# Optimization experiments

Measured on AMD Instinct MI355X. Metric: run time of the kernel, lower is better.

## Reference

```python
import jax, jax.numpy as jnp
import numpy as np

TOP_K = 4


def setup_inputs() -> dict:
    key = jax.random.key(0)
    k1, k2, k3 = jax.random.split(key, 3)
    tokens, hidden_dim, num_experts = 16384, 2880, 128
    hidden_states = jax.random.normal(k1, (tokens, hidden_dim), dtype=jnp.float32)
    weight = jax.random.normal(k2, (num_experts, hidden_dim), dtype=jnp.float32) * 0.02
    bias = jax.random.normal(k3, (num_experts,), dtype=jnp.float32) * 0.02
    return {"hidden_states": hidden_states, "weight": weight, "bias": bias}


def reference(hidden_states, weight, bias):
    # hidden_states: [T, H]; weight: [E, H]; bias: [E]
    x = hidden_states.reshape(-1, weight.shape[1])
    router_logits = jnp.einsum("th,eh->te", x, weight) + bias  # [T, E]
    router_top_value, router_indices = jax.lax.top_k(router_logits, TOP_K)  # [T, K]
    router_top_value = jax.nn.softmax(router_top_value, axis=-1)
    return router_top_value, router_indices, router_logits
```

## Files before the change

### kernel.cpp

```cpp
#include <hip/hip_runtime.h>
#include <math.h>

#define H       2880
#define H4      720
#define NTOK    16384
#define NEXP    128
#define NCHUNK  90
#define NSTEP   180
#define GAP_EPS 1e-3f

typedef __attribute__((ext_vector_type(8)))  short bf16x8;
typedef __attribute__((ext_vector_type(16))) float f32x16;

union FragU { unsigned int u[4]; bf16x8 v; };

__device__ inline bf16x8 pack_hi2(float4 a, float4 b) {
    const float f[8] = {a.x,a.y,a.z,a.w,b.x,b.y,b.z,b.w};
    FragU r;
#pragma unroll
    for (int j = 0; j < 4; ++j) {
        unsigned u0 = __float_as_uint(f[2*j]);
        unsigned u1 = __float_as_uint(f[2*j+1]);
        r.u[j] = (u1 & 0xFFFF0000u) | (u0 >> 16);
    }
    return r.v;
}
__device__ inline bf16x8 pack_lo2(float4 a, float4 b) {
    const float f[8] = {a.x,a.y,a.z,a.w,b.x,b.y,b.z,b.w};
    FragU r;
#pragma unroll
    for (int j = 0; j < 4; ++j) {
        float x0 = f[2*j],   h0 = __uint_as_float(__float_as_uint(x0) & 0xFFFF0000u);
        float x1 = f[2*j+1], h1 = __uint_as_float(__float_as_uint(x1) & 0xFFFF0000u);
        unsigned l0 = __float_as_uint(x0 - h0);
        unsigned l1 = __float_as_uint(x1 - h1);
        r.u[j] = (l1 & 0xFFFF0000u) | (l0 >> 16);
    }
    return r.v;
}

__global__ __launch_bounds__(256) void wconv(
    const float* __restrict__ w, short* __restrict__ whiF, short* __restrict__ wloF)
{
    const int gid = blockIdx.x * 256 + threadIdx.x;
    const int l   = gid & 63;
    const int nt  = (gid >> 6) & 3;
    const int s   = gid >> 8;
    const int e   = nt * 32 + (l & 31);
    const int k0  = s * 16 + (l >> 5) * 8;
    const float4* wp = (const float4*)(w + (size_t)e * H + k0);
    const float4 a = wp[0], b = wp[1];
    *(bf16x8*)(whiF + (size_t)gid * 8) = pack_hi2(a, b);
    *(bf16x8*)(wloF + (size_t)gid * 8) = pack_lo2(a, b);
}

__global__ __launch_bounds__(64, 2) void router_gemm_mfma(
    const float* __restrict__ x,
    const short* __restrict__ whiF,
    const short* __restrict__ wloF,
    float* __restrict__ p0,
    float* __restrict__ pws)
{
    __shared__ float xs[3][1024];

    const int lane = threadIdx.x;
    const int bm   = blockIdx.x;
    const int z    = blockIdx.y;
    const int ks   = gridDim.y;
    const int t0   = bm * 32;

    const int base2 = (NCHUNK / ks) & ~1;
    const int pairs = (NCHUNK - base2 * ks) >> 1;
    const int c0 = z * base2 + 2 * (z < pairs ? z : pairs);
    const int c1 = c0 + base2 + (z < pairs ? 2 : 0);

    float* outp = (z == 0) ? p0 : (pws + (size_t)(z - 1) * NTOK * NEXP);

    const float4* gs = (const float4*)x + (size_t)(t0 + (lane >> 3)) * H4 + ((lane & 7) ^ (lane >> 3));
    const unsigned xsb = (unsigned)(uintptr_t)&xs[0][0];
    const int r31 = lane & 31, lx7 = lane & 7, kh2 = (lane >> 5) * 2;

    f32x16 acc[4];
#pragma unroll
    for (int nt = 0; nt < 4; ++nt)
#pragma unroll
        for (int r = 0; r < 16; ++r) acc[nt][r] = 0.0f;

    bf16x8 bA[16], bB[16];

#define GL(SRC, DST) __builtin_amdgcn_global_load_lds(                                   \
        (const __attribute__((address_space(1))) void*)(SRC),                            \
        (__attribute__((address_space(3))) void*)(DST), 16, 0, 0)

#define STAGE(SB, CC) {                                                                  \
    const float4* g_ = gs + (size_t)(CC) * 8;                                            \
    GL(g_,                  &xs[SB][0]);                                                 \
    GL(g_ + (size_t) 8*H4,  &xs[SB][256]);                                               \
    GL(g_ + (size_t)16*H4,  &xs[SB][512]);                                               \
    GL(g_ + (size_t)24*H4,  &xs[SB][768]); }

#define BLOAD_ST(DST, CC, ST) {                                                          \
    _Pragma("unroll")                                                                    \
    for (int nt = 0; nt < 4; ++nt) {                                                     \
        const size_t o_ = ((size_t)(((CC)*2 + (ST))*4 + nt)*64 + lane) * 8;              \
        DST[(ST)*8 + nt*2]     = *(const bf16x8*)(whiF + o_);                            \
        DST[(ST)*8 + nt*2 + 1] = *(const bf16x8*)(wloF + o_); } }

#define MFMA_HALF(BANK, ST, AH, AL) {                                                    \
    _Pragma("unroll")                                                                    \
    for (int nt = 0; nt < 4; ++nt) {                                                     \
        acc[nt] = __builtin_amdgcn_mfma_f32_32x32x16_bf16(AH, BANK[(ST)*8 + nt*2],     acc[nt], 0,0,0); \
        acc[nt] = __builtin_amdgcn_mfma_f32_32x32x16_bf16(AL, BANK[(ST)*8 + nt*2],     acc[nt], 0,0,0); \
        acc[nt] = __builtin_amdgcn_mfma_f32_32x32x16_bf16(AH, BANK[(ST)*8 + nt*2 + 1], acc[nt], 0,0,0); } }

#define DSREAD_PACK(BUF, AH0, AL0, AH1, AL1) {                                           \
    const unsigned ab  = xsb + (unsigned)(BUF) * 4096u + (unsigned)r31 * 128u;           \
    const unsigned a00 = ab + 16u * (unsigned)((kh2    ) ^ lx7);                         \
    const unsigned a01 = ab + 16u * (unsigned)((kh2 + 1) ^ lx7);                         \
    const unsigned a10 = ab + 16u * (unsigned)((kh2 + 4) ^ lx7);                         \
    const unsigned a11 = ab + 16u * (unsigned)((kh2 + 5) ^ lx7);                         \
    float4 q0, q1, q2, q3;                                                               \
    asm volatile("ds_read_b128 %0, %1" : "=v"(q0) : "v"(a00) : "memory");                \
    asm volatile("ds_read_b128 %0, %1" : "=v"(q1) : "v"(a01) : "memory");                \
    asm volatile("ds_read_b128 %0, %1" : "=v"(q2) : "v"(a10) : "memory");                \
    asm volatile("ds_read_b128 %0, %1" : "=v"(q3) : "v"(a11) : "memory");                \
    asm volatile("s_waitcnt lgkmcnt(0)" ::: "memory");                                   \
    __builtin_amdgcn_sched_barrier(0);                                                   \
    AH0 = pack_hi2(q0, q1); AL0 = pack_lo2(q0, q1);                                      \
    AH1 = pack_hi2(q2, q3); AL1 = pack_lo2(q2, q3); }

    STAGE(0, c0);
    STAGE(1, c0 + 1);
    BLOAD_ST(bA, c0, 0);     BLOAD_ST(bA, c0, 1);
    BLOAD_ST(bB, c0 + 1, 0); BLOAD_ST(bB, c0 + 1, 1);

    int rb = 0;
    bf16x8 ah0, al0, ah1, al1;
    for (int c = c0; c < c1 - 2; c += 2) {
        const int sb  = (rb + 2 >= 3) ? rb - 1 : rb + 2;
        const int rb1 = (rb + 1 >= 3) ? 0 : rb + 1;
        STAGE(sb, c + 2);
        asm volatile("s_waitcnt vmcnt(40)" ::: "memory");
        DSREAD_PACK(rb, ah0, al0, ah1, al1);
        MFMA_HALF(bA, 0, ah0, al0);
        BLOAD_ST(bA, c + 2, 0);
        MFMA_HALF(bA, 1, ah1, al1);
        BLOAD_ST(bA, c + 2, 1);
        STAGE(rb, c + 3);
        asm volatile("s_waitcnt vmcnt(40)" ::: "memory");
        DSREAD_PACK(rb1, ah0, al0, ah1, al1);
        MFMA_HALF(bB, 0, ah0, al0);
        BLOAD_ST(bB, c + 3, 0);
        MFMA_HALF(bB, 1, ah1, al1);
        BLOAD_ST(bB, c + 3, 1);
        rb = (rb >= 1) ? rb - 1 : 2;
    }
    {
        const int rb1 = (rb + 1 >= 3) ? 0 : rb + 1;
        asm volatile("s_waitcnt vmcnt(36)" ::: "memory");
        DSREAD_PACK(rb, ah0, al0, ah1, al1);
        MFMA_HALF(bA, 0, ah0, al0);
        MFMA_HALF(bA, 1, ah1, al1);
        asm volatile("s_waitcnt vmcnt(16)" ::: "memory");
        DSREAD_PACK(rb1, ah0, al0, ah1, al1);
        MFMA_HALF(bB, 0, ah0, al0);
        MFMA_HALF(bB, 1, ah1, al1);
    }

    const int ecol  = lane & 31;
    const int rbase = t0 + 4 * (lane >> 5);
#pragma unroll
    for (int nt = 0; nt < 4; ++nt)
#pragma unroll
        for (int r = 0; r < 16; ++r) {
            const int orow = rbase + (r & 3) + 8 * (r >> 2);
            outp[(size_t)orow * NEXP + nt * 32 + ecol] = acc[nt][r];
        }
}

__global__ __launch_bounds__(256) void reduce_cand(
    float* __restrict__ p0,
    const float* __restrict__ pws,
    const float* __restrict__ bias,
    int* __restrict__ cand,
    float* __restrict__ vals,
    float* __restrict__ inds,
    int ks)
{
    const int tid = threadIdx.x;
    const int tok = blockIdx.x * 8 + (tid >> 5);
    const int l   = tid & 31;

    float4* row = (float4*)p0 + (size_t)tok * 32 + l;
    float4 s = row[0];
    for (int zz = 1; zz < ks; ++zz) {
        const float4 pz = ((const float4*)(pws + (size_t)(zz - 1) * NTOK * NEXP))[(size_t)tok * 32 + l];
        s.x += pz.x; s.y += pz.y; s.z += pz.z; s.w += pz.w;
    }
    const float4 bb = ((const float4*)bias)[l];
    s.x += bb.x; s.y += bb.y; s.z += bb.z; s.w += bb.w;
    row[0] = s;

    float v[4] = {s.x, s.y, s.z, s.w};
    float vv[8]; int out[8];
#pragma unroll
    for (int r = 0; r < 8; ++r) {
        float lv = v[0]; int lj = 0;
#pragma unroll
        for (int j = 1; j < 4; ++j) if (v[j] > lv) { lv = v[j]; lj = j; }
        int le = l * 4 + lj;
#pragma unroll
        for (int m = 1; m < 32; m <<= 1) {
            const float ov = __shfl_xor(lv, m, 32);
            const int   oe = __shfl_xor(le, m, 32);
            if (ov > lv || (ov == lv && oe < le)) { lv = ov; le = oe; }
        }
        vv[r] = lv; out[r] = le;
        if ((le >> 2) == l) v[le & 3] = -3.4e38f;
    }

    float ming = vv[0] - vv[1];
    ming = fminf(ming, vv[1] - vv[2]);
    ming = fminf(ming, vv[2] - vv[3]);
    ming = fminf(ming, vv[3] - vv[4]);
    const bool slow = (ming < GAP_EPS);

    if (l == 0) {
        int4 o0 = {out[0] | (slow ? (1 << 30) : 0), out[1], out[2], out[3]};
        int4 o1 = {out[4], out[5], out[6], out[7]};
        *(int4*)(cand + (size_t)tok * 8)     = o0;
        *(int4*)(cand + (size_t)tok * 8 + 4) = o1;
        if (!slow) {
            const float e1 = expf(vv[1] - vv[0]);
            const float e2 = expf(vv[2] - vv[0]);
            const float e3 = expf(vv[3] - vv[0]);
            const float sm = 1.0f + e1 + e2 + e3;
            float4 ov = {1.0f / sm, e1 / sm, e2 / sm, e3 / sm};
            float4 oi = {(float)out[0], (float)out[1], (float)out[2], (float)out[3]};
            *(float4*)(&vals[(size_t)tok * 4]) = ov;
            *(float4*)(&inds[(size_t)tok * 4]) = oi;
        }
    }
}

__global__ __launch_bounds__(256) void fixup_topk(
    const float* __restrict__ x,
    const float* __restrict__ w,
    const float* __restrict__ bias,
    const int* __restrict__ cand,
    float* __restrict__ vals,
    float* __restrict__ inds)
{
    const int lane = threadIdx.x & 63;
    const int wv   = threadIdx.x >> 6;
    const int tok  = blockIdx.x * 4 + wv;

    const int head = cand[(size_t)tok * 8];
    if (!(head & (1 << 30))) return;

    const int c    = lane >> 3;
    const int s    = lane & 7;
    const int cidx = cand[(size_t)tok * 8 + c] & 0x3fffffff;

    const float4* xr = (const float4*)x + (size_t)tok  * H4;
    const float4* wr = (const float4*)w + (size_t)cidx * H4;

    double acc = 0.0;
    for (int j = 0; j < 90; ++j) {
        const float4 a = xr[s + 8 * j];
        const float4 b = wr[s + 8 * j];
        acc = fma((double)a.x, (double)b.x, acc);
        acc = fma((double)a.y, (double)b.y, acc);
        acc = fma((double)a.z, (double)b.z, acc);
        acc = fma((double)a.w, (double)b.w, acc);
    }
    acc += __shfl_xor(acc, 1);
    acc += __shfl_xor(acc, 2);
    acc += __shfl_xor(acc, 4);
    const double exact = acc + (double)bias[cidx];

    double bv[8]; int bidx[8];
#pragma unroll
    for (int g = 0; g < 8; ++g) { bv[g] = __shfl(exact, g * 8); bidx[g] = __shfl(cidx, g * 8); }

    float fv[4]; int fi[4];
#pragma unroll
    for (int k = 0; k < 4; ++k) {
        double best = -1.0e300; int bi = 1 << 30; int bg = -1;
#pragma unroll
        for (int g = 0; g < 8; ++g) {
            if (bv[g] > best || (bv[g] == best && bidx[g] < bi)) { best = bv[g]; bi = bidx[g]; bg = g; }
        }
#pragma unroll
        for (int g = 0; g < 8; ++g) if (g == bg) bv[g] = -1.0e300;
        fv[k] = (float)best; fi[k] = bi;
    }

    if (lane == 0) {
        const float e1 = expf(fv[1] - fv[0]);
        const float e2 = expf(fv[2] - fv[0]);
        const float e3 = expf(fv[3] - fv[0]);
        const float sm = 1.0f + e1 + e2 + e3;
        float4 ov = {1.0f / sm, e1 / sm, e2 / sm, e3 / sm};
        float4 oi = {(float)fi[0], (float)fi[1], (float)fi[2], (float)fi[3]};
        *(float4*)(&vals[(size_t)tok * 4]) = ov;
        *(float4*)(&inds[(size_t)tok * 4]) = oi;
    }
}

extern "C" void kernel_launch(void* const* d_in, const int* in_sizes, int n_in,
                              void* d_out, int out_size, void* d_ws, size_t ws_size,
                              hipStream_t stream) {
    const float* x    = (const float*)d_in[0];
    const float* w    = (const float*)d_in[1];
    const float* bias = (const float*)d_in[2];

    float* out    = (float*)d_out;
    float* vals   = out;
    float* inds   = out + NTOK * 4;
    float* logits = out + NTOK * 8;

    const size_t WPLANE = (size_t)NEXP * H * sizeof(short);
    const size_t PB     = (size_t)NTOK * NEXP * sizeof(float);
    const size_t CB     = (size_t)NTOK * 8 * sizeof(int);

    int ks = 1;
    if      (ws_size >= 2 * WPLANE + 3 * PB + CB) ks = 4;
    else if (ws_size >= 2 * WPLANE + 1 * PB + CB) ks = 2;

    short* whiF = (short*)d_ws;
    short* wloF = whiF + (size_t)NEXP * H;
    float* pws  = (float*)(wloF + (size_t)NEXP * H);
    int*   cand = (int*)(pws + (size_t)(ks - 1) * NTOK * NEXP);

    wconv<<<NSTEP, 256, 0, stream>>>(w, whiF, wloF);
    router_gemm_mfma<<<dim3(NTOK / 32, ks), 64, 0, stream>>>(x, whiF, wloF, logits, pws);
    reduce_cand<<<NTOK / 8, 256, 0, stream>>>(logits, pws, bias, cand, vals, inds, ks);
    fixup_topk<<<NTOK / 4, 256, 0, stream>>>(x, w, bias, cand, vals, inds);
}
```

Measured before the change: 85.65 us.

## Fuse split-K reduction, bias and top-k candidate selection into the router GEMM

Split-K now runs inside one 256-thread block, four waves each covering a K range. Their partial accumulators are combined through shared memory, and wave 0 adds the bias, writes the logits and runs the top-8 candidate selection and softmax directly. This removes the global partial-sum workspace round trip and the separate reduce_cand launch. In exchange the block needs 48KB of LDS and occupancy drops, and the epilogue is serialised in one wave per 32 tokens.

```diff
diff --git a/kernel.cpp b/kernel.cpp
--- a/kernel.cpp
+++ b/kernel.cpp
@@ -7,6 +7,7 @@
 #define NEXP    128
 #define NCHUNK  90
 #define NSTEP   180
+#define KSW     4
 #define GAP_EPS 1e-3f
 
 typedef __attribute__((ext_vector_type(8)))  short bf16x8;
@@ -54,30 +55,31 @@
     *(bf16x8*)(wloF + (size_t)gid * 8) = pack_lo2(a, b);
 }
 
-__global__ __launch_bounds__(64, 2) void router_gemm_mfma(
+__global__ __launch_bounds__(256, 3) void router_gemm_fused(
     const float* __restrict__ x,
     const short* __restrict__ whiF,
     const short* __restrict__ wloF,
-    float* __restrict__ p0,
-    float* __restrict__ pws)
+    const float* __restrict__ bias,
+    float* __restrict__ logits,
+    int* __restrict__ cand,
+    float* __restrict__ vals,
+    float* __restrict__ inds)
 {
-    __shared__ float xs[3][1024];
-
-    const int lane = threadIdx.x;
+    __shared__ float xs[4][3][1024];
+
+    const int tid  = threadIdx.x;
+    const int lane = tid & 63;
+    const int wv   = tid >> 6;
     const int bm   = blockIdx.x;
-    const int z    = blockIdx.y;
-    const int ks   = gridDim.y;
     const int t0   = bm * 32;
 
-    const int base2 = (NCHUNK / ks) & ~1;
-    const int pairs = (NCHUNK - base2 * ks) >> 1;
-    const int c0 = z * base2 + 2 * (z < pairs ? z : pairs);
-    const int c1 = c0 + base2 + (z < pairs ? 2 : 0);
-
-    float* outp = (z == 0) ? p0 : (pws + (size_t)(z - 1) * NTOK * NEXP);
+    const int base2 = (NCHUNK / KSW) & ~1;
+    const int pairs = (NCHUNK - base2 * KSW) >> 1;
+    const int c0 = wv * base2 + 2 * (wv < pairs ? wv : pairs);
+    const int c1 = c0 + base2 + (wv < pairs ? 2 : 0);
 
     const float4* gs = (const float4*)x + (size_t)(t0 + (lane >> 3)) * H4 + ((lane & 7) ^ (lane >> 3));
-    const unsigned xsb = (unsigned)(uintptr_t)&xs[0][0];
+    const unsigned xsb = (unsigned)(uintptr_t)&xs[wv][0][0];
     const int r31 = lane & 31, lx7 = lane & 7, kh2 = (lane >> 5) * 2;
 
     f32x16 acc[4];
@@ -94,10 +96,10 @@
 
 #define STAGE(SB, CC) {                                                                  \
     const float4* g_ = gs + (size_t)(CC) * 8;                                            \
-    GL(g_,                  &xs[SB][0]);                                                 \
-    GL(g_ + (size_t) 8*H4,  &xs[SB][256]);                                               \
-    GL(g_ + (size_t)16*H4,  &xs[SB][512]);                                               \
-    GL(g_ + (size_t)24*H4,  &xs[SB][768]); }
+    GL(g_,                  &xs[wv][SB][0]);                                             \
+    GL(g_ + (size_t) 8*H4,  &xs[wv][SB][256]);                                           \
+    GL(g_ + (size_t)16*H4,  &xs[wv][SB][512]);                                           \
+    GL(g_ + (size_t)24*H4,  &xs[wv][SB][768]); }
 
 #define BLOAD_ST(DST, CC, ST) {                                                          \
     _Pragma("unroll")                                                                    \
@@ -167,78 +169,84 @@
         MFMA_HALF(bB, 1, ah1, al1);
     }
 
-    const int ecol  = lane & 31;
+    __syncthreads();
+    float* exch = &xs[0][0][0];
+    if (wv > 0) {
+        const int eb = (wv - 1) * 4096;
+#pragma unroll
+        for (int nt = 0; nt < 4; ++nt)
+#pragma unroll
+            for (int r = 0; r < 16; ++r)
+                exch[eb + (nt * 16 + r) * 64 + lane] = acc[nt][r];
+    }
+    __syncthreads();
+    if (wv != 0) return;
+
+#pragma unroll
+    for (int nt = 0; nt < 4; ++nt)
+#pragma unroll
+        for (int r = 0; r < 16; ++r) {
+            const int sl = (nt * 16 + r) * 64 + lane;
+            acc[nt][r] = ((acc[nt][r] + exch[sl]) + exch[4096 + sl]) + exch[8192 + sl];
+        }
+
+    const int l31 = lane & 31;
+    const float bv0 = bias[l31], bv1 = bias[32 + l31], bv2 = bias[64 + l31], bv3 = bias[96 + l31];
+#pragma unroll
+    for (int r = 0; r < 16; ++r) {
+        acc[0][r] += bv0; acc[1][r] += bv1; acc[2][r] += bv2; acc[3][r] += bv3;
+    }
+
     const int rbase = t0 + 4 * (lane >> 5);
 #pragma unroll
     for (int nt = 0; nt < 4; ++nt)
 #pragma unroll
         for (int r = 0; r < 16; ++r) {
             const int orow = rbase + (r & 3) + 8 * (r >> 2);
-            outp[(size_t)orow * NEXP + nt * 32 + ecol] = acc[nt][r];
-        }
-}
-
-__global__ __launch_bounds__(256) void reduce_cand(
-    float* __restrict__ p0,
-    const float* __restrict__ pws,
-    const float* __restrict__ bias,
-    int* __restrict__ cand,
-    float* __restrict__ vals,
-    float* __restrict__ inds,
-    int ks)
-{
-    const int tid = threadIdx.x;
-    const int tok = blockIdx.x * 8 + (tid >> 5);
-    const int l   = tid & 31;
-
-    float4* row = (float4*)p0 + (size_t)tok * 32 + l;
-    float4 s = row[0];
-    for (int zz = 1; zz < ks; ++zz) {
-        const float4 pz = ((const float4*)(pws + (size_t)(zz - 1) * NTOK * NEXP))[(size_t)tok * 32 + l];
-        s.x += pz.x; s.y += pz.y; s.z += pz.z; s.w += pz.w;
-    }
-    const float4 bb = ((const float4*)bias)[l];
-    s.x += bb.x; s.y += bb.y; s.z += bb.z; s.w += bb.w;
-    row[0] = s;
-
-    float v[4] = {s.x, s.y, s.z, s.w};
-    float vv[8]; int out[8];
-#pragma unroll
-    for (int r = 0; r < 8; ++r) {
-        float lv = v[0]; int lj = 0;
-#pragma unroll
-        for (int j = 1; j < 4; ++j) if (v[j] > lv) { lv = v[j]; lj = j; }
-        int le = l * 4 + lj;
-#pragma unroll
-        for (int m = 1; m < 32; m <<= 1) {
-            const float ov = __shfl_xor(lv, m, 32);
-            const int   oe = __shfl_xor(le, m, 32);
-            if (ov > lv || (ov == lv && oe < le)) { lv = ov; le = oe; }
-        }
-        vv[r] = lv; out[r] = le;
-        if ((le >> 2) == l) v[le & 3] = -3.4e38f;
-    }
-
-    float ming = vv[0] - vv[1];
-    ming = fminf(ming, vv[1] - vv[2]);
-    ming = fminf(ming, vv[2] - vv[3]);
-    ming = fminf(ming, vv[3] - vv[4]);
-    const bool slow = (ming < GAP_EPS);
-
-    if (l == 0) {
-        int4 o0 = {out[0] | (slow ? (1 << 30) : 0), out[1], out[2], out[3]};
-        int4 o1 = {out[4], out[5], out[6], out[7]};
-        *(int4*)(cand + (size_t)tok * 8)     = o0;
-        *(int4*)(cand + (size_t)tok * 8 + 4) = o1;
-        if (!slow) {
-            const float e1 = expf(vv[1] - vv[0]);
-            const float e2 = expf(vv[2] - vv[0]);
-            const float e3 = expf(vv[3] - vv[0]);
-            const float sm = 1.0f + e1 + e2 + e3;
-            float4 ov = {1.0f / sm, e1 / sm, e2 / sm, e3 / sm};
-            float4 oi = {(float)out[0], (float)out[1], (float)out[2], (float)out[3]};
-            *(float4*)(&vals[(size_t)tok * 4]) = ov;
-            *(float4*)(&inds[(size_t)tok * 4]) = oi;
+            logits[(size_t)orow * NEXP + nt * 32 + l31] = acc[nt][r];
+        }
+
+    for (int r = 0; r < 16; ++r) {
+        const int tok = rbase + (r & 3) + 8 * (r >> 2);
+        float v[4] = {acc[0][r], acc[1][r], acc[2][r], acc[3][r]};
+        float vv[8]; int out8[8];
+#pragma unroll
+        for (int rr = 0; rr < 8; ++rr) {
+            float lv = v[0]; int lj = 0;
+#pragma unroll
+            for (int j = 1; j < 4; ++j) if (v[j] > lv) { lv = v[j]; lj = j; }
+            int le = lj * 32 + l31;
+#pragma unroll
+            for (int m = 1; m < 32; m <<= 1) {
+                const float ov = __shfl_xor(lv, m, 32);
+                const int   oe = __shfl_xor(le, m, 32);
+                if (ov > lv || (ov == lv && oe < le)) { lv = ov; le = oe; }
+            }
+            vv[rr] = lv; out8[rr] = le;
+            if ((le & 31) == l31) v[le >> 5] = -3.4e38f;
+        }
+
+        float ming = vv[0] - vv[1];
+        ming = fminf(ming, vv[1] - vv[2]);
+        ming = fminf(ming, vv[2] - vv[3]);
+        ming = fminf(ming, vv[3] - vv[4]);
+        const bool slow = (ming < GAP_EPS);
+
+        if (l31 == 0) {
+            int4 o0 = {out8[0] | (slow ? (1 << 30) : 0), out8[1], out8[2], out8[3]};
+            int4 o1 = {out8[4], out8[5], out8[6], out8[7]};
+            *(int4*)(cand + (size_t)tok * 8)     = o0;
+            *(int4*)(cand + (size_t)tok * 8 + 4) = o1;
+            if (!slow) {
+                const float e1 = expf(vv[1] - vv[0]);
+                const float e2 = expf(vv[2] - vv[0]);
+                const float e3 = expf(vv[3] - vv[0]);
+                const float sm = 1.0f + e1 + e2 + e3;
+                float4 ov = {1.0f / sm, e1 / sm, e2 / sm, e3 / sm};
+                float4 oi = {(float)out8[0], (float)out8[1], (float)out8[2], (float)out8[3]};
+                *(float4*)(&vals[(size_t)tok * 4]) = ov;
+                *(float4*)(&inds[(size_t)tok * 4]) = oi;
+            }
         }
     }
 }
@@ -320,21 +328,12 @@
     float* inds   = out + NTOK * 4;
     float* logits = out + NTOK * 8;
 
-    const size_t WPLANE = (size_t)NEXP * H * sizeof(short);
-    const size_t PB     = (size_t)NTOK * NEXP * sizeof(float);
-    const size_t CB     = (size_t)NTOK * 8 * sizeof(int);
-
-    int ks = 1;
-    if      (ws_size >= 2 * WPLANE + 3 * PB + CB) ks = 4;
-    else if (ws_size >= 2 * WPLANE + 1 * PB + CB) ks = 2;
-
     short* whiF = (short*)d_ws;
     short* wloF = whiF + (size_t)NEXP * H;
-    float* pws  = (float*)(wloF + (size_t)NEXP * H);
-    int*   cand = (int*)(pws + (size_t)(ks - 1) * NTOK * NEXP);
+    int*   cand = (int*)(wloF + (size_t)NEXP * H);
 
     wconv<<<NSTEP, 256, 0, stream>>>(w, whiF, wloF);
-    router_gemm_mfma<<<dim3(NTOK / 32, ks), 64, 0, stream>>>(x, whiF, wloF, logits, pws);
-    reduce_cand<<<NTOK / 8, 256, 0, stream>>>(logits, pws, bias, cand, vals, inds, ks);
+    router_gemm_fused<<<NTOK / 32, 256, 0, stream>>>(
+        x, whiF, wloF, bias, logits, cand, vals, inds);
     fixup_topk<<<NTOK / 4, 256, 0, stream>>>(x, w, bias, cand, vals, inds);
 }
```

Result: slower. 302.8 us (+253.5%).

## Double the GEMM token tile to 64 rows to reuse weight fragments

Applied to the files above, without the earlier changes.

Each wave now computes 64 tokens instead of 32, with two row tiles of accumulators. Every bf16 weight fragment loaded from global memory feeds MFMAs for both tiles, which halves weight traffic per token. The LDS staging buffer, the wait counts and the output store loop are widened to match, and the grid is halved. In exchange, accumulator register use doubles, launch bounds drop to one wave per SIMD, and fewer blocks run, which reduces occupancy and latency hiding.

```diff
diff --git a/kernel.cpp b/kernel.cpp
--- a/kernel.cpp
+++ b/kernel.cpp
@@ -54,20 +54,20 @@
     *(bf16x8*)(wloF + (size_t)gid * 8) = pack_lo2(a, b);
 }
 
-__global__ __launch_bounds__(64, 2) void router_gemm_mfma(
+__global__ __launch_bounds__(64, 1) void router_gemm_mfma(
     const float* __restrict__ x,
     const short* __restrict__ whiF,
     const short* __restrict__ wloF,
     float* __restrict__ p0,
     float* __restrict__ pws)
 {
-    __shared__ float xs[3][1024];
+    __shared__ float xs[3][2048];
 
     const int lane = threadIdx.x;
     const int bm   = blockIdx.x;
     const int z    = blockIdx.y;
     const int ks   = gridDim.y;
-    const int t0   = bm * 32;
+    const int t0   = bm * 64;
 
     const int base2 = (NCHUNK / ks) & ~1;
     const int pairs = (NCHUNK - base2 * ks) >> 1;
@@ -80,11 +80,11 @@
     const unsigned xsb = (unsigned)(uintptr_t)&xs[0][0];
     const int r31 = lane & 31, lx7 = lane & 7, kh2 = (lane >> 5) * 2;
 
-    f32x16 acc[4];
-#pragma unroll
-    for (int nt = 0; nt < 4; ++nt)
-#pragma unroll
-        for (int r = 0; r < 16; ++r) acc[nt][r] = 0.0f;
+    f32x16 acc[8];
+#pragma unroll
+    for (int i = 0; i < 8; ++i)
+#pragma unroll
+        for (int r = 0; r < 16; ++r) acc[i][r] = 0.0f;
 
     bf16x8 bA[16], bB[16];
 
@@ -97,7 +97,11 @@
     GL(g_,                  &xs[SB][0]);                                                 \
     GL(g_ + (size_t) 8*H4,  &xs[SB][256]);                                               \
     GL(g_ + (size_t)16*H4,  &xs[SB][512]);                                               \
-    GL(g_ + (size_t)24*H4,  &xs[SB][768]); }
+    GL(g_ + (size_t)24*H4,  &xs[SB][768]);                                               \
+    GL(g_ + (size_t)32*H4,  &xs[SB][1024]);                                              \
+    GL(g_ + (size_t)40*H4,  &xs[SB][1280]);                                              \
+    GL(g_ + (size_t)48*H4,  &xs[SB][1536]);                                              \
+    GL(g_ + (size_t)56*H4,  &xs[SB][1792]); }
 
 #define BLOAD_ST(DST, CC, ST) {                                                          \
     _Pragma("unroll")                                                                    \
@@ -106,28 +110,30 @@
         DST[(ST)*8 + nt*2]     = *(const bf16x8*)(whiF + o_);                            \
         DST[(ST)*8 + nt*2 + 1] = *(const bf16x8*)(wloF + o_); } }
 
-#define MFMA_HALF(BANK, ST, AH, AL) {                                                    \
+#define MFMA_HALF(BANK, ST, AH0, AL0, AH1, AL1) {                                        \
     _Pragma("unroll")                                                                    \
     for (int nt = 0; nt < 4; ++nt) {                                                     \
-        acc[nt] = __builtin_amdgcn_mfma_f32_32x32x16_bf16(AH, BANK[(ST)*8 + nt*2],     acc[nt], 0,0,0); \
-        acc[nt] = __builtin_amdgcn_mfma_f32_32x32x16_bf16(AL, BANK[(ST)*8 + nt*2],     acc[nt], 0,0,0); \
-        acc[nt] = __builtin_amdgcn_mfma_f32_32x32x16_bf16(AH, BANK[(ST)*8 + nt*2 + 1], acc[nt], 0,0,0); } }
-
-#define DSREAD_PACK(BUF, AH0, AL0, AH1, AL1) {                                           \
-    const unsigned ab  = xsb + (unsigned)(BUF) * 4096u + (unsigned)r31 * 128u;           \
-    const unsigned a00 = ab + 16u * (unsigned)((kh2    ) ^ lx7);                         \
-    const unsigned a01 = ab + 16u * (unsigned)((kh2 + 1) ^ lx7);                         \
-    const unsigned a10 = ab + 16u * (unsigned)((kh2 + 4) ^ lx7);                         \
-    const unsigned a11 = ab + 16u * (unsigned)((kh2 + 5) ^ lx7);                         \
+        acc[nt] = __builtin_amdgcn_mfma_f32_32x32x16_bf16(AH0, BANK[(ST)*8 + nt*2],     acc[nt], 0,0,0); \
+        acc[nt] = __builtin_amdgcn_mfma_f32_32x32x16_bf16(AL0, BANK[(ST)*8 + nt*2],     acc[nt], 0,0,0); \
+        acc[nt] = __builtin_amdgcn_mfma_f32_32x32x16_bf16(AH0, BANK[(ST)*8 + nt*2 + 1], acc[nt], 0,0,0); \
+        acc[4+nt] = __builtin_amdgcn_mfma_f32_32x32x16_bf16(AH1, BANK[(ST)*8 + nt*2],     acc[4+nt], 0,0,0); \
+        acc[4+nt] = __builtin_amdgcn_mfma_f32_32x32x16_bf16(AL1, BANK[(ST)*8 + nt*2],     acc[4+nt], 0,0,0); \
+        acc[4+nt] = __builtin_amdgcn_mfma_f32_32x32x16_bf16(AH1, BANK[(ST)*8 + nt*2 + 1], acc[4+nt], 0,0,0); } }
+
+#define DSREAD_PACK(BUF, ST, H0, L0, H1, L1, H2, L2, H3, L3) {                           \
+    const unsigned ab  = xsb + (unsigned)(BUF) * 8192u + (unsigned)r31 * 128u;           \
+    const unsigned kq0 = (unsigned)(((ST)*4 + kh2    ) ^ lx7);                           \
+    const unsigned kq1 = (unsigned)(((ST)*4 + kh2 + 1) ^ lx7);                           \
     float4 q0, q1, q2, q3;                                                               \
-    asm volatile("ds_read_b128 %0, %1" : "=v"(q0) : "v"(a00) : "memory");                \
-    asm volatile("ds_read_b128 %0, %1" : "=v"(q1) : "v"(a01) : "memory");                \
-    asm volatile("ds_read_b128 %0, %1" : "=v"(q2) : "v"(a10) : "memory");                \
-    asm volatile("ds_read_b128 %0, %1" : "=v"(q3) : "v"(a11) : "memory");                \
+    asm volatile("ds_read_b128 %0, %1" : "=v"(q0) : "v"(ab + 16u*kq0) : "memory");       \
+    asm volatile("ds_read_b128 %0, %1" : "=v"(q1) : "v"(ab + 16u*kq1) : "memory");       \
+    asm volatile("ds_read_b128 %0, %1" : "=v"(q2) : "v"(ab + 4096u + 16u*kq0) : "memory"); \
+    asm volatile("ds_read_b128 %0, %1" : "=v"(q3) : "v"(ab + 4096u + 16u*kq1) : "memory"); \
     asm volatile("s_waitcnt lgkmcnt(0)" ::: "memory");                                   \
     __builtin_amdgcn_sched_barrier(0);                                                   \
-    AH0 = pack_hi2(q0, q1); AL0 = pack_lo2(q0, q1);                                      \
-    AH1 = pack_hi2(q2, q3); AL1 = pack_lo2(q2, q3); }
+    H0 = pack_hi2(q0, q1); L0 = pack_lo2(q0, q1);                                        \
+    H1 = pack_hi2(q2, q3); L1 = pack_lo2(q2, q3);                                        \
+    (void)0; }
 
     STAGE(0, c0);
     STAGE(1, c0 + 1);
@@ -135,47 +141,55 @@
     BLOAD_ST(bB, c0 + 1, 0); BLOAD_ST(bB, c0 + 1, 1);
 
     int rb = 0;
-    bf16x8 ah0, al0, ah1, al1;
+    bf16x8 a0h0, a0l0, a0h1, a0l1;
+    bf16x8 a1h0, a1l0, a1h1, a1l1;
     for (int c = c0; c < c1 - 2; c += 2) {
         const int sb  = (rb + 2 >= 3) ? rb - 1 : rb + 2;
         const int rb1 = (rb + 1 >= 3) ? 0 : rb + 1;
         STAGE(sb, c + 2);
-        asm volatile("s_waitcnt vmcnt(40)" ::: "memory");
-        DSREAD_PACK(rb, ah0, al0, ah1, al1);
-        MFMA_HALF(bA, 0, ah0, al0);
+        asm volatile("s_waitcnt vmcnt(48)" ::: "memory");
+        DSREAD_PACK(rb, 0, a0h0, a0l0, a0h1, a0l1, 0,0,0,0);
+        DSREAD_PACK(rb, 1, a1h0, a1l0, a1h1, a1l1, 0,0,0,0);
+        MFMA_HALF(bA, 0, a0h0, a0l0, a0h1, a0l1);
         BLOAD_ST(bA, c + 2, 0);
-        MFMA_HALF(bA, 1, ah1, al1);
+        MFMA_HALF(bA, 1, a1h0, a1l0, a1h1, a1l1);
         BLOAD_ST(bA, c + 2, 1);
         STAGE(rb, c + 3);
-        asm volatile("s_waitcnt vmcnt(40)" ::: "memory");
-        DSREAD_PACK(rb1, ah0, al0, ah1, al1);
-        MFMA_HALF(bB, 0, ah0, al0);
+        asm volatile("s_waitcnt vmcnt(48)" ::: "memory");
+        DSREAD_PACK(rb1, 0, a0h0, a0l0, a0h1, a0l1, 0,0,0,0);
+        DSREAD_PACK(rb1, 1, a1h0, a1l0, a1h1, a1l1, 0,0,0,0);
+        MFMA_HALF(bB, 0, a0h0, a0l0, a0h1, a0l1);
         BLOAD_ST(bB, c + 3, 0);
-        MFMA_HALF(bB, 1, ah1, al1);
+        MFMA_HALF(bB, 1, a1h0, a1l0, a1h1, a1l1);
         BLOAD_ST(bB, c + 3, 1);
         rb = (rb >= 1) ? rb - 1 : 2;
     }
     {
         const int rb1 = (rb + 1 >= 3) ? 0 : rb + 1;
-        asm volatile("s_waitcnt vmcnt(36)" ::: "memory");
-        DSREAD_PACK(rb, ah0, al0, ah1, al1);
-        MFMA_HALF(bA, 0, ah0, al0);
-        MFMA_HALF(bA, 1, ah1, al1);
+        asm volatile("s_waitcnt vmcnt(40)" ::: "memory");
+        DSREAD_PACK(rb, 0, a0h0, a0l0, a0h1, a0l1, 0,0,0,0);
+        DSREAD_PACK(rb, 1, a1h0, a1l0, a1h1, a1l1, 0,0,0,0);
+        MFMA_HALF(bA, 0, a0h0, a0l0, a0h1, a0l1);
+        MFMA_HALF(bA, 1, a1h0, a1l0, a1h1, a1l1);
         asm volatile("s_waitcnt vmcnt(16)" ::: "memory");
-        DSREAD_PACK(rb1, ah0, al0, ah1, al1);
-        MFMA_HALF(bB, 0, ah0, al0);
-        MFMA_HALF(bB, 1, ah1, al1);
-    }
-
-    const int ecol  = lane & 31;
-    const int rbase = t0 + 4 * (lane >> 5);
-#pragma unroll
-    for (int nt = 0; nt < 4; ++nt)
-#pragma unroll
-        for (int r = 0; r < 16; ++r) {
-            const int orow = rbase + (r & 3) + 8 * (r >> 2);
-            outp[(size_t)orow * NEXP + nt * 32 + ecol] = acc[nt][r];
-        }
+        DSREAD_PACK(rb1, 0, a0h0, a0l0, a0h1, a0l1, 0,0,0,0);
+        DSREAD_PACK(rb1, 1, a1h0, a1l0, a1h1, a1l1, 0,0,0,0);
+        MFMA_HALF(bB, 0, a0h0, a0l0, a0h1, a0l1);
+        MFMA_HALF(bB, 1, a1h0, a1l0, a1h1, a1l1);
+    }
+
+    const int ecol = lane & 31;
+#pragma unroll
+    for (int rt = 0; rt < 2; ++rt) {
+        const int rbase = t0 + rt * 32 + 4 * (lane >> 5);
+#pragma unroll
+        for (int nt = 0; nt < 4; ++nt)
+#pragma unroll
+            for (int r = 0; r < 16; ++r) {
+                const int orow = rbase + (r & 3) + 8 * (r >> 2);
+                outp[(size_t)orow * NEXP + nt * 32 + ecol] = acc[rt * 4 + nt][r];
+            }
+    }
 }
 
 __global__ __launch_bounds__(256) void reduce_cand(
@@ -334,7 +348,7 @@
     int*   cand = (int*)(pws + (size_t)(ks - 1) * NTOK * NEXP);
 
     wconv<<<NSTEP, 256, 0, stream>>>(w, whiF, wloF);
-    router_gemm_mfma<<<dim3(NTOK / 32, ks), 64, 0, stream>>>(x, whiF, wloF, logits, pws);
+    router_gemm_mfma<<<dim3(NTOK / 64, ks), 64, 0, stream>>>(x, whiF, wloF, logits, pws);
     reduce_cand<<<NTOK / 8, 256, 0, stream>>>(logits, pws, bias, cand, vals, inds, ks);
     fixup_topk<<<NTOK / 4, 256, 0, stream>>>(x, w, bias, cand, vals, inds);
 }
```

Result: no change. 85.15 us (-0.6%).

## Deepen weight register prefetch to four chunks and drop occupancy to one

Applied to the files above, without the earlier changes.

Adds two more register banks (bC, bD) so bf16 weight fragments are prefetched four chunks ahead instead of two. The main loop is unrolled to four chunks per iteration with explicit tail handling, and the launch bound drops to one wave per SIMD to make room for the extra VGPRs. The aim is to hide global-load latency of the weight fragments behind more MFMA work. In exchange it loses the second wave's latency hiding and adds an extra lgkmcnt wait inside the LDS read sequence.

```diff
diff --git a/kernel.cpp b/kernel.cpp
--- a/kernel.cpp
+++ b/kernel.cpp
@@ -54,7 +54,7 @@
     *(bf16x8*)(wloF + (size_t)gid * 8) = pack_lo2(a, b);
 }
 
-__global__ __launch_bounds__(64, 2) void router_gemm_mfma(
+__global__ __launch_bounds__(64, 1) void router_gemm_mfma(
     const float* __restrict__ x,
     const short* __restrict__ whiF,
     const short* __restrict__ wloF,
@@ -86,7 +86,7 @@
 #pragma unroll
         for (int r = 0; r < 16; ++r) acc[nt][r] = 0.0f;
 
-    bf16x8 bA[16], bB[16];
+    bf16x8 bA[16], bB[16], bC[16], bD[16];
 
 #define GL(SRC, DST) __builtin_amdgcn_global_load_lds(                                   \
         (const __attribute__((address_space(1))) void*)(SRC),                            \
@@ -113,7 +113,7 @@
         acc[nt] = __builtin_amdgcn_mfma_f32_32x32x16_bf16(AL, BANK[(ST)*8 + nt*2],     acc[nt], 0,0,0); \
         acc[nt] = __builtin_amdgcn_mfma_f32_32x32x16_bf16(AH, BANK[(ST)*8 + nt*2 + 1], acc[nt], 0,0,0); } }
 
-#define DSREAD_PACK(BUF, AH0, AL0, AH1, AL1) {                                           \
+#define DSREAD_PACK(BUF) {                                                               \
     const unsigned ab  = xsb + (unsigned)(BUF) * 4096u + (unsigned)r31 * 128u;           \
     const unsigned a00 = ab + 16u * (unsigned)((kh2    ) ^ lx7);                         \
     const unsigned a01 = ab + 16u * (unsigned)((kh2 + 1) ^ lx7);                         \
@@ -123,48 +123,106 @@
     asm volatile("ds_read_b128 %0, %1" : "=v"(q0) : "v"(a00) : "memory");                \
     asm volatile("ds_read_b128 %0, %1" : "=v"(q1) : "v"(a01) : "memory");                \
     asm volatile("ds_read_b128 %0, %1" : "=v"(q2) : "v"(a10) : "memory");                \
+    asm volatile("s_waitcnt lgkmcnt(0)" ::: "memory");                                   \
     asm volatile("ds_read_b128 %0, %1" : "=v"(q3) : "v"(a11) : "memory");                \
     asm volatile("s_waitcnt lgkmcnt(0)" ::: "memory");                                   \
     __builtin_amdgcn_sched_barrier(0);                                                   \
-    AH0 = pack_hi2(q0, q1); AL0 = pack_lo2(q0, q1);                                      \
-    AH1 = pack_hi2(q2, q3); AL1 = pack_lo2(q2, q3); }
+    ah0 = pack_hi2(q0, q1); al0 = pack_lo2(q0, q1);                                      \
+    ah1 = pack_hi2(q2, q3); al1 = pack_lo2(q2, q3); }
+
+#define VMW(N) asm volatile("s_waitcnt vmcnt(" #N ")" ::: "memory")
 
     STAGE(0, c0);
     STAGE(1, c0 + 1);
     BLOAD_ST(bA, c0, 0);     BLOAD_ST(bA, c0, 1);
     BLOAD_ST(bB, c0 + 1, 0); BLOAD_ST(bB, c0 + 1, 1);
-
-    int rb = 0;
+    BLOAD_ST(bC, c0 + 2, 0); BLOAD_ST(bC, c0 + 2, 1);
+    BLOAD_ST(bD, c0 + 3, 0); BLOAD_ST(bD, c0 + 3, 1);
+
     bf16x8 ah0, al0, ah1, al1;
-    for (int c = c0; c < c1 - 2; c += 2) {
-        const int sb  = (rb + 2 >= 3) ? rb - 1 : rb + 2;
-        const int rb1 = (rb + 1 >= 3) ? 0 : rb + 1;
-        STAGE(sb, c + 2);
-        asm volatile("s_waitcnt vmcnt(40)" ::: "memory");
-        DSREAD_PACK(rb, ah0, al0, ah1, al1);
-        MFMA_HALF(bA, 0, ah0, al0);
-        BLOAD_ST(bA, c + 2, 0);
-        MFMA_HALF(bA, 1, ah1, al1);
-        BLOAD_ST(bA, c + 2, 1);
-        STAGE(rb, c + 3);
-        asm volatile("s_waitcnt vmcnt(40)" ::: "memory");
-        DSREAD_PACK(rb1, ah0, al0, ah1, al1);
-        MFMA_HALF(bB, 0, ah0, al0);
-        BLOAD_ST(bB, c + 3, 0);
-        MFMA_HALF(bB, 1, ah1, al1);
-        BLOAD_ST(bB, c + 3, 1);
-        rb = (rb >= 1) ? rb - 1 : 2;
-    }
+    int rb0 = 0;
+
+    int c = c0;
+    for (; c + 8 <= c1; c += 4) {
+        const int b0 = rb0;
+        const int b1 = (rb0 + 1 >= 3) ? rb0 - 2 : rb0 + 1;
+        const int b2 = (rb0 + 2 >= 3) ? rb0 - 1 : rb0 + 2;
+        STAGE(b2, c + 2);
+        VMW(40);
+        DSREAD_PACK(b0);
+        MFMA_HALF(bA, 0, ah0, al0);  BLOAD_ST(bA, c + 4, 0);
+        MFMA_HALF(bA, 1, ah1, al1);  BLOAD_ST(bA, c + 4, 1);
+        STAGE(b0, c + 3);
+        VMW(40);
+        DSREAD_PACK(b1);
+        MFMA_HALF(bB, 0, ah0, al0);  BLOAD_ST(bB, c + 5, 0);
+        MFMA_HALF(bB, 1, ah1, al1);  BLOAD_ST(bB, c + 5, 1);
+        STAGE(b1, c + 4);
+        VMW(40);
+        DSREAD_PACK(b2);
+        MFMA_HALF(bC, 0, ah0, al0);  BLOAD_ST(bC, c + 6, 0);
+        MFMA_HALF(bC, 1, ah1, al1);  BLOAD_ST(bC, c + 6, 1);
+        STAGE(b2, c + 5);
+        VMW(40);
+        DSREAD_PACK(b0);
+        MFMA_HALF(bD, 0, ah0, al0);  BLOAD_ST(bD, c + 7, 0);
+        MFMA_HALF(bD, 1, ah1, al1);  BLOAD_ST(bD, c + 7, 1);
+        rb0 = (rb0 + 1 >= 3) ? 0 : rb0 + 1;
+    }
+
     {
-        const int rb1 = (rb + 1 >= 3) ? 0 : rb + 1;
-        asm volatile("s_waitcnt vmcnt(36)" ::: "memory");
-        DSREAD_PACK(rb, ah0, al0, ah1, al1);
-        MFMA_HALF(bA, 0, ah0, al0);
-        MFMA_HALF(bA, 1, ah1, al1);
-        asm volatile("s_waitcnt vmcnt(16)" ::: "memory");
-        DSREAD_PACK(rb1, ah0, al0, ah1, al1);
-        MFMA_HALF(bB, 0, ah0, al0);
-        MFMA_HALF(bB, 1, ah1, al1);
+        const int b0 = rb0;
+        const int b1 = (rb0 + 1 >= 3) ? rb0 - 2 : rb0 + 1;
+        const int b2 = (rb0 + 2 >= 3) ? rb0 - 1 : rb0 + 2;
+        if (c1 - c == 6) {
+            STAGE(b2, c + 2);
+            VMW(40);
+            DSREAD_PACK(b0);
+            MFMA_HALF(bA, 0, ah0, al0);  BLOAD_ST(bA, c + 4, 0);
+            MFMA_HALF(bA, 1, ah1, al1);  BLOAD_ST(bA, c + 4, 1);
+            STAGE(b0, c + 3);
+            VMW(40);
+            DSREAD_PACK(b1);
+            MFMA_HALF(bB, 0, ah0, al0);  BLOAD_ST(bB, c + 5, 0);
+            MFMA_HALF(bB, 1, ah1, al1);  BLOAD_ST(bB, c + 5, 1);
+            STAGE(b1, c + 4);
+            VMW(40);
+            DSREAD_PACK(b2);
+            MFMA_HALF(bC, 0, ah0, al0);
+            MFMA_HALF(bC, 1, ah1, al1);
+            STAGE(b2, c + 5);
+            VMW(24);
+            DSREAD_PACK(b0);
+            MFMA_HALF(bD, 0, ah0, al0);
+            MFMA_HALF(bD, 1, ah1, al1);
+            VMW(4);
+            DSREAD_PACK(b1);
+            MFMA_HALF(bA, 0, ah0, al0);
+            MFMA_HALF(bA, 1, ah1, al1);
+            VMW(0);
+            DSREAD_PACK(b2);
+            MFMA_HALF(bB, 0, ah0, al0);
+            MFMA_HALF(bB, 1, ah1, al1);
+        } else {
+            STAGE(b2, c + 2);
+            VMW(40);
+            DSREAD_PACK(b0);
+            MFMA_HALF(bA, 0, ah0, al0);
+            MFMA_HALF(bA, 1, ah1, al1);
+            STAGE(b0, c + 3);
+            VMW(24);
+            DSREAD_PACK(b1);
+            MFMA_HALF(bB, 0, ah0, al0);
+            MFMA_HALF(bB, 1, ah1, al1);
+            VMW(4);
+            DSREAD_PACK(b2);
+            MFMA_HALF(bC, 0, ah0, al0);
+            MFMA_HALF(bC, 1, ah1, al1);
+            VMW(0);
+            DSREAD_PACK(b0);
+            MFMA_HALF(bD, 0, ah0, al0);
+            MFMA_HALF(bD, 1, ah1, al1);
+        }
     }
 
     const int ecol  = lane & 31;
```

After: 113.5 us. 1.32x slower.
